# Performance work log

Hardware: AMD Instinct MI355X
Metric: run time of the kernel (lower is better)

Reference implementation:

```python
import jax, jax.numpy as jnp
import numpy as np

B = 128
NHEAD = 16
D_MODEL = 512
D_IN = 256  # each of f_* and f_*_out; concat -> 512
N_ATOM = 128


def _scopes():
    lens = np.array([96 + (i % 33) for i in range(B)], dtype=np.int64)  # max == 128 == N_ATOM
    starts_a = np.concatenate([[1], 1 + np.cumsum(lens)[:-1]]).astype(np.int64)
    nb = 2 * lens
    starts_b = np.concatenate([[1], 1 + np.cumsum(nb)[:-1]]).astype(np.int64)
    return lens, starts_a, nb, starts_b


def setup_inputs() -> dict:
    key = jax.random.key(0)
    ks = jax.random.split(key, 10)
    lens, starts_a, nb, starts_b = _scopes()
    Na = int(1 + lens.sum())   # 14279 (row 0 is padding)
    Nb = int(1 + nb.sum())     # 28557 (bond 0 is padding)
    f_atoms = jax.random.normal(ks[0], (Na, D_IN), jnp.float32)
    f_bonds = jax.random.normal(ks[1], (Nb, D_IN), jnp.float32)
    f_atoms_out = jax.random.normal(ks[2], (Na, D_IN), jnp.float32)
    f_bonds_out = jax.random.normal(ks[3], (Nb, D_IN), jnp.float32)
    b2a = jax.random.randint(ks[4], (Nb,), 0, 96, jnp.int64 if jax.config.jax_enable_x64 else jnp.int32)
    b2revb = jax.random.randint(ks[5], (Nb,), 0, Nb, b2a.dtype)
    a_scope = jnp.stack([jnp.asarray(starts_a), jnp.asarray(lens)], axis=1)
    b_scope = jnp.stack([jnp.asarray(starts_b), jnp.asarray(nb)], axis=1)
    W_atom = jax.random.normal(ks[6], (2 * D_IN, D_MODEL), jnp.float32) * 0.02
    b_atom = jnp.zeros((D_MODEL,), jnp.float32)
    W_bond = jax.random.normal(ks[7], (2 * D_IN, NHEAD), jnp.float32) * 0.02
    b_bond = jnp.zeros((NHEAD,), jnp.float32)
    return {"f_atoms": f_atoms, "f_bonds": f_bonds, "f_atoms_out": f_atoms_out,
            "f_bonds_out": f_bonds_out, "b2a": b2a, "b2revb": b2revb,
            "a_scope": a_scope, "b_scope": b_scope, "n_atom": N_ATOM,
            "W_atom": W_atom, "b_atom": b_atom, "W_bond": W_bond, "b_bond": b_bond}


def reference(f_atoms, f_bonds, f_atoms_out, f_bonds_out, b2a, b2revb,
              a_scope, b_scope, n_atom, W_atom, b_atom, W_bond, b_bond):
    Bsz = a_scope.shape[0]
    # atom embedding: concat + linear, drop padding row 0, pad per-molecule -> [n_atom, B, d]
    atoms = jnp.concatenate([f_atoms, f_atoms_out], axis=1) @ W_atom + b_atom  # [Na, d]
    starts_a, lens_a = a_scope[:, 0], a_scope[:, 1]
    pos = jnp.arange(n_atom)
    valid = pos[None, :] < lens_a[:, None]                       # [B, n_atom]
    gidx = jnp.where(valid, starts_a[:, None] + pos[None, :], 0)  # safe gather idx
    atoms_pad = jnp.where(valid[..., None], atoms[gidx], 0.0)     # [B, n_atom, d]
    atoms_emb = atoms_pad.transpose(1, 0, 2)                      # [n_atom, B, d] (batch_first=False)
    # bond embedding -> scatter into dense pairwise matrix
    bonds = jnp.concatenate([f_bonds, f_bonds_out], axis=1) @ W_bond + b_bond  # [Nb, nhead]
    Nb = bonds.shape[0]
    starts_b = b_scope[:, 0]
    mol = jnp.searchsorted(starts_b, jnp.arange(Nb), side='right') - 1  # molecule id per bond (-1 for pad bond 0)
    offset = jnp.maximum(mol, 0) * (n_atom * n_atom)
    idx = b2a + b2a[b2revb] * n_atom + offset                     # flat index into [B*n_atom*n_atom]
    flat = jnp.zeros((Bsz * n_atom * n_atom, bonds.shape[1]), bonds.dtype).at[idx].set(bonds)
    apairs = flat.reshape(Bsz, n_atom, n_atom, -1)                # [B, n_atom, n_atom, nhead]
    padding_mask = ~valid                                         # [B, n_atom], True = pad
    apairs = jnp.where(padding_mask[:, None, :, None], -jnp.inf, apairs)
    apairs = apairs.transpose(0, 3, 1, 2)                         # [B, nhead, n_atom, n_atom]
    return atoms_emb, apairs, padding_mask
```

## Files before the change

### kernel.cpp

```cpp
#include <hip/hip_runtime.h>
#include <math.h>

#define NEG_BIG (-1e30f)

typedef __attribute__((ext_vector_type(8))) short short8;
typedef __attribute__((ext_vector_type(4))) float floatx4;

__device__ __forceinline__ unsigned short f2bf(float x) {
    unsigned u = __float_as_uint(x);
    unsigned r = (u + 0x7fffu + ((u >> 16) & 1u)) >> 16;
    return (unsigned short)r;
}
__device__ __forceinline__ float bf2f(unsigned short h) {
    return __uint_as_float(((unsigned)h) << 16);
}

__global__ void k_init(int* __restrict__ w, int n) {
    int t = blockIdx.x * 256 + threadIdx.x;
    if (t < n) w[t] = -1;
}

__global__ void k_prepWa(const float* __restrict__ W, short* __restrict__ H,
                         short* __restrict__ M, short* __restrict__ L) {
    int t = blockIdx.x * 256 + threadIdx.x;
    int n = t >> 9, k = t & 511;
    float x = W[(size_t)k * 512 + n];
    unsigned short h0 = f2bf(x); float r1 = x - bf2f(h0);
    unsigned short h1 = f2bf(r1); float r2 = r1 - bf2f(h1);
    unsigned short h2 = f2bf(r2);
    H[t] = (short)h0; M[t] = (short)h1; L[t] = (short)h2;
}

__global__ void k_prepWb(const float* __restrict__ Wb, short* __restrict__ Wbt) {
    int t = blockIdx.x * 256 + threadIdx.x;
    int h = t >> 9, k = t & 511;
    Wbt[t] = (short)f2bf(Wb[(size_t)k * 16 + h]);
}

__global__ __launch_bounds__(256) void k_atoms_mfma(
    const float* __restrict__ fA, const float* __restrict__ fAo,
    const int* __restrict__ a_scope,
    const short* __restrict__ WH, const short* __restrict__ WM, const short* __restrict__ WL,
    const float* __restrict__ bias, float* __restrict__ out, int Bmol)
{
    __shared__ short A_s[3][128 * 40];
    __shared__ short B_s[3][128 * 40];
    __shared__ int rs[128];

    const int tid = threadIdx.x;
    const int n0 = blockIdx.x * 128;
    const int mol = blockIdx.y;

    if (tid < 128) {
        int len = a_scope[2 * mol + 1];
        rs[tid] = (tid < len) ? (a_scope[2 * mol] + tid) : -1;
    }
    const int wid = tid >> 6, lane = tid & 63;
    const int wm = (wid >> 1) * 64, wn = (wid & 1) * 64;
    const int quad = lane >> 4, l16 = lane & 15;

    floatx4 acc[4][4];
#pragma unroll
    for (int i = 0; i < 4; i++)
#pragma unroll
        for (int j = 0; j < 4; j++) acc[i][j] = (floatx4){0.f, 0.f, 0.f, 0.f};

    const int ar = tid >> 1;
    const int ak = (tid & 1) * 16;
    __syncthreads();
    const int asrc = rs[ar];

    for (int k0 = 0; k0 < 512; k0 += 32) {
        float x[16];
        if (asrc >= 0) {
            int kg = k0 + ak;
            const float* p = (kg < 256) ? (fA + (size_t)asrc * 256 + kg)
                                        : (fAo + (size_t)asrc * 256 + (kg - 256));
#pragma unroll
            for (int i = 0; i < 4; i++) {
                float4 v = ((const float4*)p)[i];
                x[i * 4 + 0] = v.x; x[i * 4 + 1] = v.y;
                x[i * 4 + 2] = v.z; x[i * 4 + 3] = v.w;
            }
        } else {
#pragma unroll
            for (int i = 0; i < 16; i++) x[i] = 0.f;
        }
        size_t goff = (size_t)(n0 + ar) * 512 + k0 + ak;
        short8 bh0 = *(const short8*)(WH + goff);
        short8 bh1 = *(const short8*)(WH + goff + 8);
        short8 bm0 = *(const short8*)(WM + goff);
        short8 bm1 = *(const short8*)(WM + goff + 8);
        short8 bl0 = *(const short8*)(WL + goff);
        short8 bl1 = *(const short8*)(WL + goff + 8);

        short8 a00, a01, a10, a11, a20, a21;
#pragma unroll
        for (int i = 0; i < 8; i++) {
            unsigned short h0 = f2bf(x[i]); float r1 = x[i] - bf2f(h0);
            unsigned short h1 = f2bf(r1);   float r2 = r1 - bf2f(h1);
            a00[i] = (short)h0; a10[i] = (short)h1; a20[i] = (short)f2bf(r2);
        }
#pragma unroll
        for (int i = 0; i < 8; i++) {
            float xx = x[8 + i];
            unsigned short h0 = f2bf(xx); float r1 = xx - bf2f(h0);
            unsigned short h1 = f2bf(r1); float r2 = r1 - bf2f(h1);
            a01[i] = (short)h0; a11[i] = (short)h1; a21[i] = (short)f2bf(r2);
        }

        __syncthreads();
        const int abase = ar * 40 + ak;
        *(short8*)&A_s[0][abase] = a00; *(short8*)&A_s[0][abase + 8] = a01;
        *(short8*)&A_s[1][abase] = a10; *(short8*)&A_s[1][abase + 8] = a11;
        *(short8*)&A_s[2][abase] = a20; *(short8*)&A_s[2][abase + 8] = a21;
        *(short8*)&B_s[0][abase] = bh0; *(short8*)&B_s[0][abase + 8] = bh1;
        *(short8*)&B_s[1][abase] = bm0; *(short8*)&B_s[1][abase + 8] = bm1;
        *(short8*)&B_s[2][abase] = bl0; *(short8*)&B_s[2][abase + 8] = bl1;
        __syncthreads();

        short8 af[3][4];
#pragma unroll
        for (int ti = 0; ti < 4; ti++) {
            int off = (wm + ti * 16 + l16) * 40 + quad * 8;
            af[0][ti] = *(const short8*)&A_s[0][off];
            af[1][ti] = *(const short8*)&A_s[1][off];
            af[2][ti] = *(const short8*)&A_s[2][off];
        }
#pragma unroll
        for (int tj = 0; tj < 4; tj++) {
            int off = (wn + tj * 16 + l16) * 40 + quad * 8;
            short8 b0 = *(const short8*)&B_s[0][off];
            short8 b1 = *(const short8*)&B_s[1][off];
            short8 b2 = *(const short8*)&B_s[2][off];
#pragma unroll
            for (int ti = 0; ti < 4; ti++) {
                floatx4 c = acc[ti][tj];
                c = __builtin_amdgcn_mfma_f32_16x16x32_bf16(af[0][ti], b0, c, 0, 0, 0);
                c = __builtin_amdgcn_mfma_f32_16x16x32_bf16(af[0][ti], b1, c, 0, 0, 0);
                c = __builtin_amdgcn_mfma_f32_16x16x32_bf16(af[1][ti], b0, c, 0, 0, 0);
                c = __builtin_amdgcn_mfma_f32_16x16x32_bf16(af[0][ti], b2, c, 0, 0, 0);
                c = __builtin_amdgcn_mfma_f32_16x16x32_bf16(af[1][ti], b1, c, 0, 0, 0);
                c = __builtin_amdgcn_mfma_f32_16x16x32_bf16(af[2][ti], b0, c, 0, 0, 0);
                acc[ti][tj] = c;
            }
        }
    }

#pragma unroll
    for (int tj = 0; tj < 4; tj++) {
        int n = n0 + wn + tj * 16 + l16;
        float bv = bias[n];
#pragma unroll
        for (int ti = 0; ti < 4; ti++) {
#pragma unroll
            for (int r = 0; r < 4; r++) {
                int pos = wm + ti * 16 + quad * 4 + r;
                bool valid = rs[pos] >= 0;
                float v = valid ? (acc[ti][tj][r] + bv) : 0.f;
                out[((size_t)pos * Bmol + mol) * 512 + n] = v;
            }
        }
    }
}

__global__ __launch_bounds__(256) void k_bonds_mfma(
    const float* __restrict__ fB, const float* __restrict__ fBo,
    const short* __restrict__ Wbt, const float* __restrict__ bb_,
    float* __restrict__ bonds, int Nb)
{
    __shared__ short feat[64 * 136];
    __shared__ short wb[16 * 512];

    const int tid = threadIdx.x;
    const int j0 = blockIdx.x * 64;

    for (int c = tid; c < 1024; c += 256) {
        int h = c >> 6, cc = c & 63;
        short8 v = *(const short8*)(Wbt + h * 512 + cc * 8);
        *(short8*)&wb[h * 512 + (((cc + h) & 63) * 8)] = v;
    }

    const int wid = tid >> 6, lane = tid & 63;
    const int quad = lane >> 4, l16 = lane & 15;
    floatx4 acc = (floatx4){0.f, 0.f, 0.f, 0.f};

    const int fr = tid >> 2;
    const int fs = (tid & 3) * 32;
    const int j = j0 + fr;

    for (int k0 = 0; k0 < 512; k0 += 128) {
        float x[32];
        if (j < Nb) {
            const float* p = (k0 < 256) ? (fB + (size_t)j * 256 + k0 + fs)
                                        : (fBo + (size_t)j * 256 + (k0 - 256) + fs);
#pragma unroll
            for (int i = 0; i < 8; i++) {
                float4 v = ((const float4*)p)[i];
                x[i * 4 + 0] = v.x; x[i * 4 + 1] = v.y;
                x[i * 4 + 2] = v.z; x[i * 4 + 3] = v.w;
            }
        } else {
#pragma unroll
            for (int i = 0; i < 32; i++) x[i] = 0.f;
        }
        __syncthreads();
#pragma unroll
        for (int c = 0; c < 4; c++) {
            short8 s;
#pragma unroll
            for (int i = 0; i < 8; i++) s[i] = (short)f2bf(x[c * 8 + i]);
            *(short8*)&feat[fr * 136 + fs + c * 8] = s;
        }
        __syncthreads();
#pragma unroll
        for (int kk = 0; kk < 4; kk++) {
            short8 a = *(const short8*)&feat[(wid * 16 + l16) * 136 + kk * 32 + quad * 8];
            int kchunk = (k0 + kk * 32 + quad * 8) >> 3;
            short8 b = *(const short8*)&wb[l16 * 512 + (((kchunk + l16) & 63) * 8)];
            acc = __builtin_amdgcn_mfma_f32_16x16x32_bf16(a, b, acc, 0, 0, 0);
        }
    }
    float bv = bb_[l16];
#pragma unroll
    for (int r = 0; r < 4; r++) {
        int jj = j0 + wid * 16 + quad * 4 + r;
        if (jj < Nb) bonds[(size_t)jj * 16 + l16] = acc[r] + bv;
    }
}

__global__ void k_scatter(const int* __restrict__ b2a, const int* __restrict__ b2revb,
                          const int* __restrict__ b_scope, int* __restrict__ winner,
                          int Nb, int Bmol)
{
    __shared__ int sb[128];
    int tid = threadIdx.x;
    if (tid < Bmol) sb[tid] = b_scope[2 * tid];
    __syncthreads();
    int j = blockIdx.x * 256 + tid;
    if (j >= Nb) return;
    int lo = 0, hi = Bmol;
    while (lo < hi) { int mid = (lo + hi) >> 1; if (sb[mid] <= j) lo = mid + 1; else hi = mid; }
    int mol = lo - 1; if (mol < 0) mol = 0;
    int p2 = b2a[j];
    int p1 = b2a[b2revb[j]];
    atomicMax(&winner[mol * 16384 + p1 * 128 + p2], j);
}

__global__ __launch_bounds__(256) void k_apairs(
    const int* __restrict__ winner, const float* __restrict__ bonds,
    const int* __restrict__ a_scope, float* __restrict__ out, int Bmol)
{
    int t = blockIdx.x * 256 + threadIdx.x;
    int b = t >> 12;
    int p1 = (t >> 5) & 127;
    int p2q = t & 31;
    int len = a_scope[2 * b + 1];
    const int4 w = ((const int4*)winner)[t];
    float* ob = out + ((size_t)b * 16 * 128 + p1) * 128 + p2q * 4;
#pragma unroll
    for (int h = 0; h < 16; h++) {
        float4 v;
        v.x = (p2q * 4 + 0 >= len) ? NEG_BIG : (w.x >= 0 ? bonds[(size_t)w.x * 16 + h] : 0.f);
        v.y = (p2q * 4 + 1 >= len) ? NEG_BIG : (w.y >= 0 ? bonds[(size_t)w.y * 16 + h] : 0.f);
        v.z = (p2q * 4 + 2 >= len) ? NEG_BIG : (w.z >= 0 ? bonds[(size_t)w.z * 16 + h] : 0.f);
        v.w = (p2q * 4 + 3 >= len) ? NEG_BIG : (w.w >= 0 ? bonds[(size_t)w.w * 16 + h] : 0.f);
        *(float4*)(ob + (size_t)h * 16384) = v;
    }
}

__global__ void k_mask(const int* __restrict__ a_scope, float* __restrict__ out, int Bmol) {
    int t = blockIdx.x * 256 + threadIdx.x;
    if (t >= Bmol * 128) return;
    int b = t >> 7, p = t & 127;
    out[t] = (p >= a_scope[2 * b + 1]) ? 1.0f : 0.0f;
}

extern "C" void kernel_launch(void* const* d_in, const int* in_sizes, int n_in,
                              void* d_out, int out_size, void* d_ws, size_t ws_size,
                              hipStream_t stream)
{
    const float* f_atoms     = (const float*)d_in[0];
    const float* f_bonds     = (const float*)d_in[1];
    const float* f_atoms_out = (const float*)d_in[2];
    const float* f_bonds_out = (const float*)d_in[3];
    const int*   b2a         = (const int*)d_in[4];
    const int*   b2revb      = (const int*)d_in[5];
    const int*   a_scope     = (const int*)d_in[6];
    const int*   b_scope     = (const int*)d_in[7];
    const float* W_atom      = (const float*)d_in[9];
    const float* b_atom      = (const float*)d_in[10];
    const float* W_bond      = (const float*)d_in[11];
    const float* b_bond      = (const float*)d_in[12];

    const int Bmol = in_sizes[6] / 2;
    const int Nb   = in_sizes[4];

    char* ws = (char*)d_ws;
    size_t off = 0;
    float* bonds_ws = (float*)(ws + off); off += ((size_t)Nb * 16 * 4 + 255) & ~(size_t)255;
    int*   winner   = (int*)(ws + off);   off += (size_t)Bmol * 16384 * 4;
    short* WH       = (short*)(ws + off); off += 512 * 512 * 2;
    short* WM       = (short*)(ws + off); off += 512 * 512 * 2;
    short* WL       = (short*)(ws + off); off += 512 * 512 * 2;
    short* Wbt      = (short*)(ws + off); off += 16 * 512 * 2;

    float* out_emb  = (float*)d_out;
    float* out_ap   = out_emb + (size_t)128 * Bmol * 512;
    float* out_mask = out_ap + (size_t)Bmol * 16 * 128 * 128;

    const int ncell = Bmol * 16384;
    hipLaunchKernelGGL(k_prepWa, dim3(1024), dim3(256), 0, stream, W_atom, WH, WM, WL);
    hipLaunchKernelGGL(k_prepWb, dim3(32), dim3(256), 0, stream, W_bond, Wbt);
    hipLaunchKernelGGL(k_init, dim3((ncell + 255) / 256), dim3(256), 0, stream, winner, ncell);
    hipLaunchKernelGGL(k_atoms_mfma, dim3(4, Bmol), dim3(256), 0, stream,
                       f_atoms, f_atoms_out, a_scope, WH, WM, WL, b_atom, out_emb, Bmol);
    hipLaunchKernelGGL(k_bonds_mfma, dim3((Nb + 63) / 64), dim3(256), 0, stream,
                       f_bonds, f_bonds_out, Wbt, b_bond, bonds_ws, Nb);
    hipLaunchKernelGGL(k_scatter, dim3((Nb + 255) / 256), dim3(256), 0, stream,
                       b2a, b2revb, b_scope, winner, Nb, Bmol);
    hipLaunchKernelGGL(k_apairs, dim3(Bmol * 4096 / 256), dim3(256), 0, stream,
                       winner, bonds_ws, a_scope, out_ap, Bmol);
    hipLaunchKernelGGL(k_mask, dim3((Bmol * 128 + 255) / 256), dim3(256), 0, stream,
                       a_scope, out_mask, Bmol);
}
```

Before: 322.7 us.

## Fuse scatter, apairs and mask into per-molecule LDS kernel; read atom weights directly

Replaces the global winner buffer (init, atomic scatter, gather) with one block per molecule that builds the 128x128 winner table in shared memory using LDS atomics, then writes the pair tensor and padding mask. This removes three launches and the global winner round trip. Separately, the atom GEMM now loads the B fragments straight from global memory instead of staging them through LDS. The pair kernel launches only 128 blocks of 512 threads, with 64KB of LDS each, so its parallelism drops. The direct global B loads may cost more memory traffic per MFMA.

Result: slower. 359.3 us (+11.3%).

```diff
diff --git a/kernel.cpp b/kernel.cpp
--- a/kernel.cpp
+++ b/kernel.cpp
@@ -13,11 +13,6 @@
 }
 __device__ __forceinline__ float bf2f(unsigned short h) {
     return __uint_as_float(((unsigned)h) << 16);
-}
-
-__global__ void k_init(int* __restrict__ w, int n) {
-    int t = blockIdx.x * 256 + threadIdx.x;
-    if (t < n) w[t] = -1;
 }
 
 __global__ void k_prepWa(const float* __restrict__ W, short* __restrict__ H,
@@ -44,7 +39,6 @@
     const float* __restrict__ bias, float* __restrict__ out, int Bmol)
 {
     __shared__ short A_s[3][128 * 40];
-    __shared__ short B_s[3][128 * 40];
     __shared__ int rs[128];
 
     const int tid = threadIdx.x;
@@ -86,14 +80,6 @@
 #pragma unroll
             for (int i = 0; i < 16; i++) x[i] = 0.f;
         }
-        size_t goff = (size_t)(n0 + ar) * 512 + k0 + ak;
-        short8 bh0 = *(const short8*)(WH + goff);
-        short8 bh1 = *(const short8*)(WH + goff + 8);
-        short8 bm0 = *(const short8*)(WM + goff);
-        short8 bm1 = *(const short8*)(WM + goff + 8);
-        short8 bl0 = *(const short8*)(WL + goff);
-        short8 bl1 = *(const short8*)(WL + goff + 8);
-
         short8 a00, a01, a10, a11, a20, a21;
 #pragma unroll
         for (int i = 0; i < 8; i++) {
@@ -114,9 +100,6 @@
         *(short8*)&A_s[0][abase] = a00; *(short8*)&A_s[0][abase + 8] = a01;
         *(short8*)&A_s[1][abase] = a10; *(short8*)&A_s[1][abase + 8] = a11;
         *(short8*)&A_s[2][abase] = a20; *(short8*)&A_s[2][abase + 8] = a21;
-        *(short8*)&B_s[0][abase] = bh0; *(short8*)&B_s[0][abase + 8] = bh1;
-        *(short8*)&B_s[1][abase] = bm0; *(short8*)&B_s[1][abase + 8] = bm1;
-        *(short8*)&B_s[2][abase] = bl0; *(short8*)&B_s[2][abase + 8] = bl1;
         __syncthreads();
 
         short8 af[3][4];
@@ -129,10 +112,10 @@
         }
 #pragma unroll
         for (int tj = 0; tj < 4; tj++) {
-            int off = (wn + tj * 16 + l16) * 40 + quad * 8;
-            short8 b0 = *(const short8*)&B_s[0][off];
-            short8 b1 = *(const short8*)&B_s[1][off];
-            short8 b2 = *(const short8*)&B_s[2][off];
+            size_t bbase = (size_t)(n0 + wn + tj * 16 + l16) * 512 + k0 + quad * 8;
+            short8 b0 = *(const short8*)(WH + bbase);
+            short8 b1 = *(const short8*)(WM + bbase);
+            short8 b2 = *(const short8*)(WL + bbase);
 #pragma unroll
             for (int ti = 0; ti < 4; ti++) {
                 floatx4 c = acc[ti][tj];
@@ -229,51 +212,67 @@
     }
 }
 
-__global__ void k_scatter(const int* __restrict__ b2a, const int* __restrict__ b2revb,
-                          const int* __restrict__ b_scope, int* __restrict__ winner,
-                          int Nb, int Bmol)
+__global__ __launch_bounds__(512) void k_pair(
+    const int* __restrict__ b2a, const int* __restrict__ b2revb,
+    const int* __restrict__ b_scope, const int* __restrict__ a_scope,
+    const float* __restrict__ bonds, float* __restrict__ out_ap,
+    float* __restrict__ out_mask, int Bmol)
 {
-    __shared__ int sb[128];
-    int tid = threadIdx.x;
-    if (tid < Bmol) sb[tid] = b_scope[2 * tid];
+    __shared__ int w[16384];
+    const int tid = threadIdx.x;
+    const int mol = blockIdx.x;
+
+#pragma unroll
+    for (int i = 0; i < 8; i++)
+        ((int4*)w)[i * 512 + tid] = make_int4(-1, -1, -1, -1);
+
+    const int bs = b_scope[2 * mol];
+    const int bc = b_scope[2 * mol + 1];
+    const int len = a_scope[2 * mol + 1];
     __syncthreads();
-    int j = blockIdx.x * 256 + tid;
-    if (j >= Nb) return;
-    int lo = 0, hi = Bmol;
-    while (lo < hi) { int mid = (lo + hi) >> 1; if (sb[mid] <= j) lo = mid + 1; else hi = mid; }
-    int mol = lo - 1; if (mol < 0) mol = 0;
-    int p2 = b2a[j];
-    int p1 = b2a[b2revb[j]];
-    atomicMax(&winner[mol * 16384 + p1 * 128 + p2], j);
-}
-
-__global__ __launch_bounds__(256) void k_apairs(
-    const int* __restrict__ winner, const float* __restrict__ bonds,
-    const int* __restrict__ a_scope, float* __restrict__ out, int Bmol)
-{
-    int t = blockIdx.x * 256 + threadIdx.x;
-    int b = t >> 12;
-    int p1 = (t >> 5) & 127;
-    int p2q = t & 31;
-    int len = a_scope[2 * b + 1];
-    const int4 w = ((const int4*)winner)[t];
-    float* ob = out + ((size_t)b * 16 * 128 + p1) * 128 + p2q * 4;
-#pragma unroll
-    for (int h = 0; h < 16; h++) {
-        float4 v;
-        v.x = (p2q * 4 + 0 >= len) ? NEG_BIG : (w.x >= 0 ? bonds[(size_t)w.x * 16 + h] : 0.f);
-        v.y = (p2q * 4 + 1 >= len) ? NEG_BIG : (w.y >= 0 ? bonds[(size_t)w.y * 16 + h] : 0.f);
-        v.z = (p2q * 4 + 2 >= len) ? NEG_BIG : (w.z >= 0 ? bonds[(size_t)w.z * 16 + h] : 0.f);
-        v.w = (p2q * 4 + 3 >= len) ? NEG_BIG : (w.w >= 0 ? bonds[(size_t)w.w * 16 + h] : 0.f);
-        *(float4*)(ob + (size_t)h * 16384) = v;
-    }
-}
-
-__global__ void k_mask(const int* __restrict__ a_scope, float* __restrict__ out, int Bmol) {
-    int t = blockIdx.x * 256 + threadIdx.x;
-    if (t >= Bmol * 128) return;
-    int b = t >> 7, p = t & 127;
-    out[t] = (p >= a_scope[2 * b + 1]) ? 1.0f : 0.0f;
+
+    for (int q = tid; q < bc; q += 512) {
+        int j = bs + q;
+        int p2 = b2a[j];
+        int p1 = b2a[b2revb[j]];
+        atomicMax(&w[p1 * 128 + p2], j);
+    }
+    if (mol == 0 && tid == 0) {
+        int p2 = b2a[0];
+        int p1 = b2a[b2revb[0]];
+        atomicMax(&w[p1 * 128 + p2], 0);
+    }
+    __syncthreads();
+
+    if (tid < 32) {
+        int p = tid * 4;
+        float4 mv;
+        mv.x = (p + 0 >= len) ? 1.0f : 0.0f;
+        mv.y = (p + 1 >= len) ? 1.0f : 0.0f;
+        mv.z = (p + 2 >= len) ? 1.0f : 0.0f;
+        mv.w = (p + 3 >= len) ? 1.0f : 0.0f;
+        *(float4*)&out_mask[mol * 128 + p] = mv;
+    }
+
+    const int p1 = tid >> 2;
+    float* ob = out_ap + ((size_t)mol * 16 * 128 + p1) * 128;
+#pragma unroll
+    for (int g = 0; g < 8; g++) {
+        int p2q = (tid & 3) + g * 4;
+        int4 wv = ((const int4*)w)[p1 * 32 + p2q];
+        int p2 = p2q * 4;
+        bool m0 = (p2 + 0 >= len), m1 = (p2 + 1 >= len);
+        bool m2 = (p2 + 2 >= len), m3 = (p2 + 3 >= len);
+#pragma unroll
+        for (int h = 0; h < 16; h++) {
+            float4 v;
+            v.x = m0 ? NEG_BIG : (wv.x >= 0 ? bonds[(size_t)wv.x * 16 + h] : 0.f);
+            v.y = m1 ? NEG_BIG : (wv.y >= 0 ? bonds[(size_t)wv.y * 16 + h] : 0.f);
+            v.z = m2 ? NEG_BIG : (wv.z >= 0 ? bonds[(size_t)wv.z * 16 + h] : 0.f);
+            v.w = m3 ? NEG_BIG : (wv.w >= 0 ? bonds[(size_t)wv.w * 16 + h] : 0.f);
+            *(float4*)(ob + (size_t)h * 16384 + p2) = v;
+        }
+    }
 }
 
 extern "C" void kernel_launch(void* const* d_in, const int* in_sizes, int n_in,
@@ -299,7 +298,6 @@
     char* ws = (char*)d_ws;
     size_t off = 0;
     float* bonds_ws = (float*)(ws + off); off += ((size_t)Nb * 16 * 4 + 255) & ~(size_t)255;
-    int*   winner   = (int*)(ws + off);   off += (size_t)Bmol * 16384 * 4;
     short* WH       = (short*)(ws + off); off += 512 * 512 * 2;
     short* WM       = (short*)(ws + off); off += 512 * 512 * 2;
     short* WL       = (short*)(ws + off); off += 512 * 512 * 2;
@@ -309,18 +307,12 @@
     float* out_ap   = out_emb + (size_t)128 * Bmol * 512;
     float* out_mask = out_ap + (size_t)Bmol * 16 * 128 * 128;
 
-    const int ncell = Bmol * 16384;
     hipLaunchKernelGGL(k_prepWa, dim3(1024), dim3(256), 0, stream, W_atom, WH, WM, WL);
     hipLaunchKernelGGL(k_prepWb, dim3(32), dim3(256), 0, stream, W_bond, Wbt);
-    hipLaunchKernelGGL(k_init, dim3((ncell + 255) / 256), dim3(256), 0, stream, winner, ncell);
     hipLaunchKernelGGL(k_atoms_mfma, dim3(4, Bmol), dim3(256), 0, stream,
                        f_atoms, f_atoms_out, a_scope, WH, WM, WL, b_atom, out_emb, Bmol);
     hipLaunchKernelGGL(k_bonds_mfma, dim3((Nb + 63) / 64), dim3(256), 0, stream,
                        f_bonds, f_bonds_out, Wbt, b_bond, bonds_ws, Nb);
-    hipLaunchKernelGGL(k_scatter, dim3((Nb + 255) / 256), dim3(256), 0, stream,
-                       b2a, b2revb, b_scope, winner, Nb, Bmol);
-    hipLaunchKernelGGL(k_apairs, dim3(Bmol * 4096 / 256), dim3(256), 0, stream,
-                       winner, bonds_ws, a_scope, out_ap, Bmol);
-    hipLaunchKernelGGL(k_mask, dim3((Bmol * 128 + 255) / 256), dim3(256), 0, stream,
-                       a_scope, out_mask, Bmol);
-}
+    hipLaunchKernelGGL(k_pair, dim3(Bmol), dim3(512), 0, stream,
+                       b2a, b2revb, b_scope, a_scope, bonds_ws, out_ap, out_mask, Bmol);
+}
```
